# Kernel tuning notes

Hardware: AMD Instinct MI355X
Metric: run time of the kernel (lower is better)

## Reference

```python
import jax, jax.numpy as jnp
import numpy as np

N, E, B = 65536, 262144, 2048   # nodes, edges, graphs
ND, ED, H, L = 32, 8, 128, 4    # node feat, edge feat, hidden, egnn layers
PE, PH, CH = 1280, 512, 512     # protein embed, protein hidden, combined hidden
EPS = 1e-8


def _seg_mean(data, ids, num):
    s = jax.ops.segment_sum(data, ids, num_segments=num)
    c = jax.ops.segment_sum(jnp.ones((data.shape[0], 1), data.dtype), ids, num_segments=num)
    return s / jnp.clip(c, 1.0)


def setup_inputs() -> dict:
    key = jax.random.key(0)
    ks = iter(jax.random.split(key, 40))

    def p(shape, scale=0.05):
        return jax.random.normal(next(ks), shape, dtype=jnp.float32) * scale

    inp = {
        "x": jax.random.normal(next(ks), (N, ND), dtype=jnp.float32),
        "pos": jax.random.normal(next(ks), (N, 3), dtype=jnp.float32),
        "edge_attr": jax.random.uniform(next(ks), (E, ED), dtype=jnp.float32),
        "protein_embedding": jax.random.normal(next(ks), (B, PE), dtype=jnp.float32),
        "edge_index": jax.random.randint(next(ks), (2, E), 0, N),
        "batch": jnp.arange(N, dtype=jnp.int64) // (N // B),
        # EGNN embeddings
        "emb_in_w": p((ND, H)), "emb_in_b": p((H,)),
        "emb_out_w": p((H, H)), "emb_out_b": p((H,)),
        # per-layer stacked params (leading dim L)
        "edge_w1": p((L, 2 * H + 1 + ED, H)), "edge_b1": p((L, H)),
        "edge_w2": p((L, H, H)), "edge_b2": p((L, H)),
        "att_w": p((L, H, 1)), "att_b": p((L, 1)),
        "coord_w1": p((L, H, H)), "coord_b1": p((L, H)),
        "coord_w2": p((L, H, 1)),  # no bias, xavier in torch impl
        "node_w1": p((L, 2 * H, H)), "node_b1": p((L, H)),
        "node_w2": p((L, H, H)), "node_b2": p((L, H)),
        # protein + combined heads
        "prot_w": p((PE, PH)), "prot_b": p((PH,)),
        "comb_w1": p((H + PH, CH)), "comb_b1": p((CH,)),
        "comb_w2": p((CH, 1)), "comb_b2": p((1,)),
    }
    return inp


def _forward(x, pos, edge_attr, protein_embedding,
             emb_in_w, emb_in_b, emb_out_w, emb_out_b,
             edge_w1, edge_b1, edge_w2, edge_b2, att_w, att_b,
             coord_w1, coord_b1, coord_w2,
             node_w1, node_b1, node_w2, node_b2,
             prot_w, prot_b, comb_w1, comb_b1, comb_w2, comb_b2,
             edge_index, batch):
    row, col = edge_index[0], edge_index[1]
    h = x @ emb_in_w + emb_in_b
    for l in range(L):
        # coord2radial (normalize=True)
        d = pos[row] - pos[col]                       # [E,3]
        radial = jnp.sum(d * d, axis=-1, keepdims=True)  # [E,1]
        d = d / (jnp.sqrt(radial) + EPS)
        # edge model with sigmoid attention gate
        e_in = jnp.concatenate([h[row], h[col], radial, edge_attr], axis=-1)
        m = jax.nn.silu(e_in @ edge_w1[l] + edge_b1[l])
        m = jax.nn.silu(m @ edge_w2[l] + edge_b2[l])
        m = m * jax.nn.sigmoid(m @ att_w[l] + att_b[l])
        # coord model (tanh=True, coords_agg='mean')
        t = jax.nn.silu(m @ coord_w1[l] + coord_b1[l])
        trans = d * jnp.tanh(t @ coord_w2[l])         # [E,3]
        pos = pos + _seg_mean(trans, row, N)
        # node model (sum aggregation, residual)
        agg = jax.ops.segment_sum(m, row, num_segments=N)
        nh = jax.nn.silu(jnp.concatenate([h, agg], axis=-1) @ node_w1[l] + node_b1[l])
        h = h + (nh @ node_w2[l] + node_b2[l])
    h = h @ emb_out_w + emb_out_b
    # global mean pool over graphs
    drug = _seg_mean(h, batch, B)                     # [B,H]
    prot = jax.nn.relu(protein_embedding @ prot_w + prot_b)  # dropout = identity (eval)
    c = jnp.concatenate([drug, prot], axis=-1)
    c = jax.nn.relu(c @ comb_w1 + comb_b1)
    logits = (c @ comb_w2 + comb_b2)[:, 0]
    return logits


def reference(x, pos, edge_attr, protein_embedding,
              emb_in_w, emb_in_b, emb_out_w, emb_out_b,
              edge_w1, edge_b1, edge_w2, edge_b2, att_w, att_b,
              coord_w1, coord_b1, coord_w2,
              node_w1, node_b1, node_w2, node_b2,
              prot_w, prot_b, comb_w1, comb_b1, comb_w2, comb_b2,
              edge_index, batch):
    logits = _forward(x, pos, edge_attr, protein_embedding,
                      emb_in_w, emb_in_b, emb_out_w, emb_out_b,
                      edge_w1, edge_b1, edge_w2, edge_b2, att_w, att_b,
                      coord_w1, coord_b1, coord_w2,
                      node_w1, node_b1, node_w2, node_b2,
                      prot_w, prot_b, comb_w1, comb_b1, comb_w2, comb_b2,
                      edge_index, batch)
    attention_weights = jnp.zeros((B, 1, 1), dtype=logits.dtype)
    return logits, attention_weights
```

## Files before the change

kernel.cpp:

```cpp
#include <hip/hip_runtime.h>
#include <math.h>


static constexpr int NN  = 65536;
static constexpr int NE  = 262144;
static constexpr int NB  = 2048;
static constexpr int NDF = 32;
static constexpr int HD  = 128;
static constexpr int NL  = 4;
static constexpr int PED = 1280;
static constexpr int PHD = 512;
static constexpr int CHD = 512;
static constexpr float EPSV = 1e-8f;

static constexpr int KK1 = 9;
static constexpr int KK2 = 4;
static constexpr int KKN1 = 8;
static constexpr int KKP = 40;
static constexpr int KKC = 20;

static constexpr int ES = 36;

typedef __attribute__((ext_vector_type(8))) short bf8_t;
typedef __attribute__((ext_vector_type(4))) float f4_t;

__device__ __forceinline__ float sigmoid_f(float x) {
  return __fdividef(1.0f, 1.0f + __expf(-x));
}
__device__ __forceinline__ float silu_f(float x) { return x * sigmoid_f(x); }

__device__ __forceinline__ ushort f2bf(float f) {
  unsigned u = __float_as_uint(f);
  u += 0x7FFFu + ((u >> 16) & 1u);
  return (ushort)(u >> 16);
}
__device__ __forceinline__ float bf2f(ushort h) {
  return __uint_as_float(((unsigned)h) << 16);
}
__device__ __forceinline__ unsigned pk2bf(float a, float b) {
  return (unsigned)f2bf(a) | ((unsigned)f2bf(b) << 16);
}

__device__ __forceinline__ void fma44(float (&acc)[4][4], const float4 a, const float4 w) {
  const float av[4] = {a.x, a.y, a.z, a.w};
  const float wv[4] = {w.x, w.y, w.z, w.w};
#pragma unroll
  for (int i = 0; i < 4; ++i)
#pragma unroll
    for (int j = 0; j < 4; ++j) acc[i][j] = fmaf(av[i], wv[j], acc[i][j]);
}


__global__ void hist_kernel(const int* __restrict__ ei, int* __restrict__ deg) {
  const int e = blockIdx.x * 256 + threadIdx.x;
  if (e < NE) atomicAdd(&deg[ei[e]], 1);
}

__global__ __launch_bounds__(1024) void scan_kernel(const int* __restrict__ deg,
                                                    int* __restrict__ row_ptr) {
  __shared__ int wsums[16];
  __shared__ int carry_s;
  const int t = threadIdx.x;
  const int lane = t & 63, wave = t >> 6;
  if (t == 0) { carry_s = 0; row_ptr[0] = 0; }
  __syncthreads();
  for (int c = 0; c < NN / 1024; ++c) {
    const int i = c * 1024 + t;
    int incl = deg[i];
#pragma unroll
    for (int d = 1; d < 64; d <<= 1) {
      const int u = __shfl_up(incl, d, 64);
      if (lane >= d) incl += u;
    }
    if (lane == 63) wsums[wave] = incl;
    __syncthreads();
    if (t == 0) {
      int a = carry_s;
#pragma unroll
      for (int w = 0; w < 16; ++w) { const int tmp = wsums[w]; wsums[w] = a; a += tmp; }
      carry_s = a;
    }
    __syncthreads();
    row_ptr[i + 1] = wsums[wave] + incl;
    __syncthreads();
  }
}

__global__ void fill_kernel(const int* __restrict__ ei, const int* __restrict__ row_ptr,
                            int* __restrict__ fill_pos, int* __restrict__ edge_ids) {
  const int e = blockIdx.x * 256 + threadIdx.x;
  if (e < NE) {
    const int n = ei[e];
    const int s = atomicAdd(&fill_pos[n], 1);
    edge_ids[row_ptr[n] + s] = e;
  }
}

__global__ void perm_kernel(const int* __restrict__ ei, const int* __restrict__ edge_ids,
                            const float* __restrict__ edge_attr,
                            int* __restrict__ rowp, int* __restrict__ colp,
                            float* __restrict__ eap) {
  const int i = blockIdx.x * 256 + threadIdx.x;
  if (i >= NE) return;
  const int e = edge_ids[i];
  rowp[i] = ei[e];
  colp[i] = ei[NE + e];
  const float4 a = *(const float4*)(edge_attr + (size_t)e * 8);
  const float4 b = *(const float4*)(edge_attr + (size_t)e * 8 + 4);
  *(float4*)(eap + (size_t)i * 8) = a;
  *(float4*)(eap + (size_t)i * 8 + 4) = b;
}

__global__ void pos_copy_kernel(const float* __restrict__ pos, float* __restrict__ pc) {
  const int n = blockIdx.x * 256 + threadIdx.x;
  if (n < NN) {
    const float4 v = make_float4(pos[(size_t)n * 3 + 0], pos[(size_t)n * 3 + 1],
                                 pos[(size_t)n * 3 + 2], 0.0f);
    *(float4*)(pc + (size_t)n * 4) = v;
  }
}


__global__ __launch_bounds__(256) void packw_kernel(
    const float* __restrict__ W, ushort* __restrict__ Wp,
    int K, int N, int KK, size_t sW, size_t sWp) {
  const int layer = blockIdx.y;
  const int NTG = N >> 4;
  const int i = blockIdx.x * 256 + threadIdx.x;
  if (i >= KK * NTG * 64) return;
  const int l = i & 63;
  const int q = i >> 6;
  const int ntg = q % NTG;
  const int kk = q / NTG;
  const int k0 = kk * 32 + ((l >> 4) * 8);
  const int n = ntg * 16 + (l & 15);
  const float* w = W + layer * sW;
  unsigned ww[4];
#pragma unroll
  for (int p = 0; p < 4; ++p) {
    const int ka = k0 + p * 2, kb = ka + 1;
    const unsigned lo = (ka < K) ? f2bf(w[(size_t)ka * N + n]) : 0;
    const unsigned hi = (kb < K) ? f2bf(w[(size_t)kb * N + n]) : 0;
    ww[p] = lo | (hi << 16);
  }
  *(uint4*)(Wp + layer * sWp + (size_t)i * 8) = make_uint4(ww[0], ww[1], ww[2], ww[3]);
}

__global__ __launch_bounds__(256) void cvt_bf_kernel(const float* __restrict__ in,
                                                     ushort* __restrict__ out, int n) {
  const int i = blockIdx.x * 256 + threadIdx.x;
  if (i * 8 >= n) return;
  const float4 v0 = *(const float4*)(in + (size_t)i * 8);
  const float4 v1 = *(const float4*)(in + (size_t)i * 8 + 4);
  *(uint4*)(out + (size_t)i * 8) =
      make_uint4(pk2bf(v0.x, v0.y), pk2bf(v0.z, v0.w), pk2bf(v1.x, v1.y), pk2bf(v1.z, v1.w));
}


__global__ __launch_bounds__(256) void geom_kernel(
    const float* __restrict__ pos_cur, const float* __restrict__ eap,
    const int* __restrict__ rowp, const int* __restrict__ colp,
    float* __restrict__ dnb, ushort* __restrict__ extra) {
  const int i = blockIdx.x * 256 + threadIdx.x;
  if (i >= NE) return;
  const int r = rowp[i], c = colp[i];
  const float4 pr = *(const float4*)(pos_cur + (size_t)r * 4);
  const float4 pc = *(const float4*)(pos_cur + (size_t)c * 4);
  const float dx = pr.x - pc.x, dy = pr.y - pc.y, dz = pr.z - pc.z;
  const float radial = dx * dx + dy * dy + dz * dz;
  const float inv = 1.0f / (sqrtf(radial) + EPSV);
  *(float4*)(dnb + (size_t)i * 4) = make_float4(dx * inv, dy * inv, dz * inv, 0.0f);
  const float4 ea0 = *(const float4*)(eap + (size_t)i * 8);
  const float4 ea1 = *(const float4*)(eap + (size_t)i * 8 + 4);
  ushort* dst = extra + (size_t)i * 32;
  *(uint4*)(dst) = make_uint4(pk2bf(radial, ea0.x), pk2bf(ea0.y, ea0.z),
                              pk2bf(ea0.w, ea1.x), pk2bf(ea1.y, ea1.z));
  *(uint4*)(dst + 8)  = make_uint4((unsigned)f2bf(ea1.w), 0, 0, 0);
  *(uint4*)(dst + 16) = make_uint4(0, 0, 0, 0);
  *(uint4*)(dst + 24) = make_uint4(0, 0, 0, 0);
}


__global__ __launch_bounds__(256) void emb_in_kernel(
    const float* __restrict__ x, const float* __restrict__ W,
    const float* __restrict__ B, float* __restrict__ h, ushort* __restrict__ hbf) {
  __shared__ float xs[NDF * ES];
  const int t = threadIdx.x;
  const int n0 = blockIdx.x * 32;
  {
    const int r = t >> 3;
    const int kq = (t & 7) * 4;
    const float4 v = *(const float4*)(x + (size_t)(n0 + r) * NDF + kq);
    xs[(kq + 0) * ES + r] = v.x;
    xs[(kq + 1) * ES + r] = v.y;
    xs[(kq + 2) * ES + r] = v.z;
    xs[(kq + 3) * ES + r] = v.w;
  }
  __syncthreads();
  const int eg = t & 7, fg = t >> 3;
  float acc[4][4] = {};
  const float* wp = W + fg * 4;
#pragma unroll
  for (int k = 0; k < NDF; ++k) {
    const float4 a = *(const float4*)&xs[k * ES + eg * 4];
    const float4 w = *(const float4*)(wp + (size_t)k * HD);
    fma44(acc, a, w);
  }
  const float4 bv = *(const float4*)(B + fg * 4);
  const float bb[4] = {bv.x, bv.y, bv.z, bv.w};
#pragma unroll
  for (int i = 0; i < 4; ++i) {
    const float4 o = make_float4(acc[i][0] + bb[0], acc[i][1] + bb[1],
                                 acc[i][2] + bb[2], acc[i][3] + bb[3]);
    *(float4*)(h + (size_t)(n0 + eg * 4 + i) * HD + fg * 4) = o;
    *(uint2*)(hbf + (size_t)(n0 + eg * 4 + i) * HD + fg * 4) =
        make_uint2(pk2bf(o.x, o.y), pk2bf(o.z, o.w));
  }
}


__global__ __launch_bounds__(256) void edge_mfma_kernel(
    const ushort* __restrict__ hbf, const ushort* __restrict__ extra,
    const int* __restrict__ rowp, const int* __restrict__ colp,
    const float* __restrict__ dnb,
    const ushort* __restrict__ W1p, const float* __restrict__ B1,
    const ushort* __restrict__ W2p, const float* __restrict__ B2,
    const float* __restrict__ AW, const float* __restrict__ AB,
    const ushort* __restrict__ CW1p, const float* __restrict__ CB1,
    const float* __restrict__ CW2,
    ushort* __restrict__ m_bf, float* __restrict__ trans_out) {
  __shared__ ushort mtileT[64 * 128];
  __shared__ int ridx[64], cidx[64];
  __shared__ float redbuf[2][64];
  __shared__ float gates[64];

  const int t = threadIdx.x;
  const int e0 = blockIdx.x * 64;
  if (t < 64) {
    ridx[t] = rowp[e0 + t];
    cidx[t] = colp[e0 + t];
  }
  __syncthreads();

  const int w = t >> 6, l = t & 63;
  const int wn = w & 1, we = w >> 1;
  const int g = l >> 4, ln = l & 15;
  const int nb = wn * 64;
  const int eb = we * 32;

  int je[2], er[2], ec[2], swz[2];
#pragma unroll
  for (int et = 0; et < 2; ++et) {
    je[et] = eb + et * 16 + ln;
    er[et] = ridx[je[et]];
    ec[et] = cidx[je[et]];
    swz[et] = (je[et] & 7) << 3;
  }

  const f4_t zf = {0.0f, 0.0f, 0.0f, 0.0f};
  f4_t acc[4][2];
#pragma unroll
  for (int mt = 0; mt < 4; ++mt)
#pragma unroll
    for (int et = 0; et < 2; ++et) acc[mt][et] = zf;

#pragma unroll
  for (int kk = 0; kk < KK1; ++kk) {
    bf8_t aw[4], be[2];
#pragma unroll
    for (int mt = 0; mt < 4; ++mt)
      aw[mt] = *(const bf8_t*)(W1p + ((size_t)(kk * 8 + wn * 4 + mt) * 64 + l) * 8);
#pragma unroll
    for (int et = 0; et < 2; ++et) {
      if (kk < 8) {
        const int idx = (kk < 4) ? er[et] : ec[et];
        be[et] = *(const bf8_t*)(hbf + (size_t)idx * HD + (kk & 3) * 32 + g * 8);
      } else {
        be[et] = *(const bf8_t*)(extra + (size_t)(e0 + je[et]) * 32 + g * 8);
      }
    }
#pragma unroll
    for (int mt = 0; mt < 4; ++mt)
#pragma unroll
      for (int et = 0; et < 2; ++et)
        acc[mt][et] = __builtin_amdgcn_mfma_f32_16x16x32_bf16(aw[mt], be[et], acc[mt][et], 0, 0, 0);
  }

  {
#pragma unroll
    for (int mt = 0; mt < 4; ++mt) {
      const int n0 = nb + mt * 16 + g * 4;
      const float4 bv = *(const float4*)(B1 + n0);
#pragma unroll
      for (int et = 0; et < 2; ++et) {
        const unsigned lo = pk2bf(silu_f(acc[mt][et][0] + bv.x), silu_f(acc[mt][et][1] + bv.y));
        const unsigned hi = pk2bf(silu_f(acc[mt][et][2] + bv.z), silu_f(acc[mt][et][3] + bv.w));
        *(uint2*)&mtileT[je[et] * HD + (n0 ^ swz[et])] = make_uint2(lo, hi);
      }
    }
  }
  __syncthreads();

  f4_t acc2[4][2];
#pragma unroll
  for (int mt = 0; mt < 4; ++mt)
#pragma unroll
    for (int et = 0; et < 2; ++et) acc2[mt][et] = zf;
#pragma unroll
  for (int kk = 0; kk < KK2; ++kk) {
    bf8_t aw[4], be[2];
#pragma unroll
    for (int mt = 0; mt < 4; ++mt)
      aw[mt] = *(const bf8_t*)(W2p + ((size_t)(kk * 8 + wn * 4 + mt) * 64 + l) * 8);
    const int nk = kk * 32 + g * 8;
#pragma unroll
    for (int et = 0; et < 2; ++et)
      be[et] = *(const bf8_t*)&mtileT[je[et] * HD + (nk ^ swz[et])];
#pragma unroll
    for (int mt = 0; mt < 4; ++mt)
#pragma unroll
      for (int et = 0; et < 2; ++et)
        acc2[mt][et] = __builtin_amdgcn_mfma_f32_16x16x32_bf16(aw[mt], be[et], acc2[mt][et], 0, 0, 0);
  }

  float m2v[4][2][4];
  {
    float p[2] = {0.0f, 0.0f};
#pragma unroll
    for (int mt = 0; mt < 4; ++mt) {
      const int n0 = nb + mt * 16 + g * 4;
      const float4 bv = *(const float4*)(B2 + n0);
      const float4 av = *(const float4*)(AW + n0);
      const float bb[4] = {bv.x, bv.y, bv.z, bv.w};
      const float aa[4] = {av.x, av.y, av.z, av.w};
#pragma unroll
      for (int et = 0; et < 2; ++et)
#pragma unroll
        for (int r = 0; r < 4; ++r) {
          const float v = silu_f(acc2[mt][et][r] + bb[r]);
          m2v[mt][et][r] = v;
          p[et] = fmaf(v, aa[r], p[et]);
        }
    }
#pragma unroll
    for (int et = 0; et < 2; ++et) {
      p[et] += __shfl_xor(p[et], 16, 64);
      p[et] += __shfl_xor(p[et], 32, 64);
    }
    if (l < 16) {
#pragma unroll
      for (int et = 0; et < 2; ++et) redbuf[wn][eb + et * 16 + l] = p[et];
    }
  }
  __syncthreads();
  if (t < 64) gates[t] = sigmoid_f(redbuf[0][t] + redbuf[1][t] + AB[0]);
  __syncthreads();

  {
    float grow[2];
#pragma unroll
    for (int et = 0; et < 2; ++et) grow[et] = gates[je[et]];
#pragma unroll
    for (int mt = 0; mt < 4; ++mt) {
      const int n0 = nb + mt * 16 + g * 4;
#pragma unroll
      for (int et = 0; et < 2; ++et) {
        const unsigned lo = pk2bf(m2v[mt][et][0] * grow[et], m2v[mt][et][1] * grow[et]);
        const unsigned hi = pk2bf(m2v[mt][et][2] * grow[et], m2v[mt][et][3] * grow[et]);
        *(uint2*)&mtileT[je[et] * HD + (n0 ^ swz[et])] = make_uint2(lo, hi);
      }
    }
  }
  __syncthreads();

  f4_t acc3[4][2];
#pragma unroll
  for (int mt = 0; mt < 4; ++mt)
#pragma unroll
    for (int et = 0; et < 2; ++et) acc3[mt][et] = zf;
#pragma unroll
  for (int kk = 0; kk < KK2; ++kk) {
    bf8_t aw[4], be[2];
#pragma unroll
    for (int mt = 0; mt < 4; ++mt)
      aw[mt] = *(const bf8_t*)(CW1p + ((size_t)(kk * 8 + wn * 4 + mt) * 64 + l) * 8);
    const int nk = kk * 32 + g * 8;
#pragma unroll
    for (int et = 0; et < 2; ++et)
      be[et] = *(const bf8_t*)&mtileT[je[et] * HD + (nk ^ swz[et])];
#pragma unroll
    for (int mt = 0; mt < 4; ++mt)
#pragma unroll
      for (int et = 0; et < 2; ++et)
        acc3[mt][et] = __builtin_amdgcn_mfma_f32_16x16x32_bf16(aw[mt], be[et], acc3[mt][et], 0, 0, 0);
  }
  {
    float q[2] = {0.0f, 0.0f};
#pragma unroll
    for (int mt = 0; mt < 4; ++mt) {
      const int n0 = nb + mt * 16 + g * 4;
      const float4 bv = *(const float4*)(CB1 + n0);
      const float4 cv = *(const float4*)(CW2 + n0);
      const float bb[4] = {bv.x, bv.y, bv.z, bv.w};
      const float cc[4] = {cv.x, cv.y, cv.z, cv.w};
#pragma unroll
      for (int et = 0; et < 2; ++et)
#pragma unroll
        for (int r = 0; r < 4; ++r)
          q[et] = fmaf(silu_f(acc3[mt][et][r] + bb[r]), cc[r], q[et]);
    }
#pragma unroll
    for (int et = 0; et < 2; ++et) {
      q[et] += __shfl_xor(q[et], 16, 64);
      q[et] += __shfl_xor(q[et], 32, 64);
    }
    if (l < 16) {
#pragma unroll
      for (int et = 0; et < 2; ++et) redbuf[wn][eb + et * 16 + l] = q[et];
    }
  }
  __syncthreads();
  if (t < 64) {
    const float s = tanhf(redbuf[0][t] + redbuf[1][t]);
    const f4_t dn = *(const f4_t*)(dnb + (size_t)(e0 + t) * 4);
    const f4_t tr = dn * s;
    *(f4_t*)(trans_out + (size_t)(e0 + t) * 4) = tr;
  }

#pragma unroll
  for (int it = 0; it < 4; ++it) {
    const int i = it * 256 + t;
    const int row = i >> 4;
    const int c8 = (i & 15) * 8;
    const uint4 v = *(const uint4*)&mtileT[row * HD + (c8 ^ ((row & 7) << 3))];
    *(uint4*)(m_bf + (size_t)(e0 + row) * HD + c8) = v;
  }
}


__global__ __launch_bounds__(256) void gather_kernel(
    const ushort* __restrict__ m_bf, const float* __restrict__ trans,
    const int* __restrict__ row_ptr,
    ushort* __restrict__ agg_bf, float* __restrict__ pos_cur) {
  const int t = threadIdx.x;
  const int wave = t >> 6, lane = t & 63;
  const int n = blockIdx.x * 4 + wave;
  const int s = row_ptr[n], e_end = row_ptr[n + 1];
  float a0 = 0.0f, a1 = 0.0f, ta = 0.0f;
  for (int i = s; i < e_end; ++i) {
    const ushort2 v = *(const ushort2*)(m_bf + (size_t)i * HD + lane * 2);
    a0 += bf2f(v.x);
    a1 += bf2f(v.y);
    if (lane < 4) ta += trans[(size_t)i * 4 + lane];
  }
  ushort2 ab;
  ab.x = f2bf(a0);
  ab.y = f2bf(a1);
  *(ushort2*)(agg_bf + (size_t)n * HD + lane * 2) = ab;
  if (lane < 3) {
    const int dg = e_end - s;
    pos_cur[(size_t)n * 4 + lane] += ta / (float)(dg > 0 ? dg : 1);
  }
}


__global__ __launch_bounds__(256) void node_mfma_kernel(
    float* __restrict__ h, const ushort* __restrict__ hbf,
    const ushort* __restrict__ agg_bf,
    const ushort* __restrict__ W1p, const float* __restrict__ B1,
    const ushort* __restrict__ W2p, const float* __restrict__ B2,
    ushort* __restrict__ hbf_out) {
  __shared__ ushort mtileT[64 * 128];
  const int t = threadIdx.x;
  const int n0blk = blockIdx.x * 64;
  const int w = t >> 6, l = t & 63;
  const int wn = w & 1, we = w >> 1;
  const int g = l >> 4, ln = l & 15;
  const int nb = wn * 64;
  const int eb = we * 32;

  int jn[2], swz[2];
#pragma unroll
  for (int et = 0; et < 2; ++et) {
    jn[et] = eb + et * 16 + ln;
    swz[et] = (jn[et] & 7) << 3;
  }

  const f4_t zf = {0.0f, 0.0f, 0.0f, 0.0f};
  f4_t acc[4][2];
#pragma unroll
  for (int mt = 0; mt < 4; ++mt)
#pragma unroll
    for (int et = 0; et < 2; ++et) acc[mt][et] = zf;

#pragma unroll
  for (int kk = 0; kk < KKN1; ++kk) {
    bf8_t aw[4], be[2];
#pragma unroll
    for (int mt = 0; mt < 4; ++mt)
      aw[mt] = *(const bf8_t*)(W1p + ((size_t)(kk * 8 + wn * 4 + mt) * 64 + l) * 8);
#pragma unroll
    for (int et = 0; et < 2; ++et) {
      const size_t base = (size_t)(n0blk + jn[et]) * HD + (kk & 3) * 32 + g * 8;
      be[et] = (kk < 4) ? *(const bf8_t*)(hbf + base) : *(const bf8_t*)(agg_bf + base);
    }
#pragma unroll
    for (int mt = 0; mt < 4; ++mt)
#pragma unroll
      for (int et = 0; et < 2; ++et)
        acc[mt][et] = __builtin_amdgcn_mfma_f32_16x16x32_bf16(aw[mt], be[et], acc[mt][et], 0, 0, 0);
  }
  {
#pragma unroll
    for (int mt = 0; mt < 4; ++mt) {
      const int n0 = nb + mt * 16 + g * 4;
      const float4 bv = *(const float4*)(B1 + n0);
#pragma unroll
      for (int et = 0; et < 2; ++et) {
        const unsigned lo = pk2bf(silu_f(acc[mt][et][0] + bv.x), silu_f(acc[mt][et][1] + bv.y));
        const unsigned hi = pk2bf(silu_f(acc[mt][et][2] + bv.z), silu_f(acc[mt][et][3] + bv.w));
        *(uint2*)&mtileT[jn[et] * HD + (n0 ^ swz[et])] = make_uint2(lo, hi);
      }
    }
  }
  __syncthreads();

  f4_t acc2[4][2];
#pragma unroll
  for (int mt = 0; mt < 4; ++mt)
#pragma unroll
    for (int et = 0; et < 2; ++et) acc2[mt][et] = zf;
#pragma unroll
  for (int kk = 0; kk < KK2; ++kk) {
    bf8_t aw[4], be[2];
#pragma unroll
    for (int mt = 0; mt < 4; ++mt)
      aw[mt] = *(const bf8_t*)(W2p + ((size_t)(kk * 8 + wn * 4 + mt) * 64 + l) * 8);
    const int nk = kk * 32 + g * 8;
#pragma unroll
    for (int et = 0; et < 2; ++et)
      be[et] = *(const bf8_t*)&mtileT[jn[et] * HD + (nk ^ swz[et])];
#pragma unroll
    for (int mt = 0; mt < 4; ++mt)
#pragma unroll
      for (int et = 0; et < 2; ++et)
        acc2[mt][et] = __builtin_amdgcn_mfma_f32_16x16x32_bf16(aw[mt], be[et], acc2[mt][et], 0, 0, 0);
  }
  {
#pragma unroll
    for (int mt = 0; mt < 4; ++mt) {
      const int n0 = nb + mt * 16 + g * 4;
      const float4 bv = *(const float4*)(B2 + n0);
#pragma unroll
      for (int et = 0; et < 2; ++et) {
        float* hp = h + (size_t)(n0blk + jn[et]) * HD + n0;
        const float4 old = *(const float4*)hp;
        float4 o;
        o.x = old.x + acc2[mt][et][0] + bv.x;
        o.y = old.y + acc2[mt][et][1] + bv.y;
        o.z = old.z + acc2[mt][et][2] + bv.z;
        o.w = old.w + acc2[mt][et][3] + bv.w;
        *(float4*)hp = o;
        *(uint2*)(hbf_out + (size_t)(n0blk + jn[et]) * HD + n0) =
            make_uint2(pk2bf(o.x, o.y), pk2bf(o.z, o.w));
      }
    }
  }
}


__global__ __launch_bounds__(256) void gemm_head_kernel(
    const ushort* __restrict__ A, const ushort* __restrict__ Wp,
    const float* __restrict__ bias, ushort* __restrict__ out,
    int lda, int KK, int NTG, int ldo, int col_off) {
  const int t = threadIdx.x;
  const int rb = blockIdx.x * 64;
  const int cb = blockIdx.y * 128;
  const int w = t >> 6, l = t & 63;
  const int wr = w >> 1, wc = w & 1;
  const int g = l >> 4, ln = l & 15;
  const int row0 = wr * 32;
  int rowA[2];
#pragma unroll
  for (int mt = 0; mt < 2; ++mt) rowA[mt] = row0 + mt * 16 + ln;

  const f4_t zf = {0.0f, 0.0f, 0.0f, 0.0f};
  f4_t acc[2][4];
#pragma unroll
  for (int mt = 0; mt < 2; ++mt)
#pragma unroll
    for (int nt = 0; nt < 4; ++nt) acc[mt][nt] = zf;

  const int ntg0 = (cb >> 4) + wc * 4;
  for (int kk = 0; kk < KK; ++kk) {
    bf8_t a[2], b[4];
#pragma unroll
    for (int mt = 0; mt < 2; ++mt)
      a[mt] = *(const bf8_t*)(A + (size_t)(rb + rowA[mt]) * lda + kk * 32 + g * 8);
#pragma unroll
    for (int nt = 0; nt < 4; ++nt)
      b[nt] = *(const bf8_t*)(Wp + ((size_t)(kk * NTG + ntg0 + nt) * 64 + l) * 8);
#pragma unroll
    for (int mt = 0; mt < 2; ++mt)
#pragma unroll
      for (int nt = 0; nt < 4; ++nt)
        acc[mt][nt] = __builtin_amdgcn_mfma_f32_16x16x32_bf16(a[mt], b[nt], acc[mt][nt], 0, 0, 0);
  }
  {
    float bn[4];
#pragma unroll
    for (int nt = 0; nt < 4; ++nt) bn[nt] = bias[cb + wc * 64 + nt * 16 + ln];
#pragma unroll
    for (int mt = 0; mt < 2; ++mt)
#pragma unroll
      for (int nt = 0; nt < 4; ++nt) {
        const int col = cb + wc * 64 + nt * 16 + ln;
#pragma unroll
        for (int r = 0; r < 4; ++r) {
          const int row = row0 + mt * 16 + g * 4 + r;
          const float v = fmaxf(acc[mt][nt][r] + bn[nt], 0.0f);
          out[(size_t)(rb + row) * ldo + col_off + col] = f2bf(v);
        }
      }
  }
}


__global__ __launch_bounds__(128) void pool_kernel(
    const float* __restrict__ h, const float* __restrict__ W,
    const float* __restrict__ B, ushort* __restrict__ c_in) {
  __shared__ float mh[HD];
  const int g = blockIdx.x, t = threadIdx.x;
  float s = 0.0f;
#pragma unroll 4
  for (int n = 0; n < 32; ++n) s += h[((size_t)g * 32 + n) * HD + t];
  mh[t] = s * (1.0f / 32.0f);
  __syncthreads();
  float acc = B[t];
#pragma unroll 4
  for (int k = 0; k < HD; ++k) acc = fmaf(mh[k], W[(size_t)k * HD + t], acc);
  c_in[(size_t)g * (HD + PHD) + t] = f2bf(acc);
}

__global__ __launch_bounds__(256) void logits_kernel(
    const ushort* __restrict__ c, const float* __restrict__ w2,
    const float* __restrict__ b2, float* __restrict__ out) {
  const int t = threadIdx.x;
  const int wave = t >> 6, lane = t & 63;
  const int r = blockIdx.x * 4 + wave;
  const ushort* cp = c + (size_t)r * CHD + lane * 8;
  const float* wp = w2 + lane * 8;
  float s = 0.0f;
#pragma unroll
  for (int j = 0; j < 8; ++j) s = fmaf(bf2f(cp[j]), wp[j], s);
#pragma unroll
  for (int off = 32; off > 0; off >>= 1) s += __shfl_down(s, off, 64);
  if (lane == 0) {
    out[r] = s + b2[0];
    out[NB + r] = 0.0f;
  }
}


extern "C" void kernel_launch(void* const* d_in, const int* in_sizes, int n_in,
                              void* d_out, int out_size, void* d_ws, size_t ws_size,
                              hipStream_t stream) {
  const float* x          = (const float*)d_in[0];
  const float* pos        = (const float*)d_in[1];
  const float* edge_attr  = (const float*)d_in[2];
  const float* pe         = (const float*)d_in[3];
  const int*   edge_index = (const int*)d_in[4];
  const float* emb_in_w   = (const float*)d_in[6];
  const float* emb_in_b   = (const float*)d_in[7];
  const float* emb_out_w  = (const float*)d_in[8];
  const float* emb_out_b  = (const float*)d_in[9];
  const float* edge_w1    = (const float*)d_in[10];
  const float* edge_b1    = (const float*)d_in[11];
  const float* edge_w2    = (const float*)d_in[12];
  const float* edge_b2    = (const float*)d_in[13];
  const float* att_w      = (const float*)d_in[14];
  const float* att_b      = (const float*)d_in[15];
  const float* coord_w1   = (const float*)d_in[16];
  const float* coord_b1   = (const float*)d_in[17];
  const float* coord_w2   = (const float*)d_in[18];
  const float* node_w1    = (const float*)d_in[19];
  const float* node_b1    = (const float*)d_in[20];
  const float* node_w2    = (const float*)d_in[21];
  const float* node_b2    = (const float*)d_in[22];
  const float* prot_w     = (const float*)d_in[23];
  const float* prot_b     = (const float*)d_in[24];
  const float* comb_w1    = (const float*)d_in[25];
  const float* comb_b1    = (const float*)d_in[26];
  const float* comb_w2    = (const float*)d_in[27];
  const float* comb_b2    = (const float*)d_in[28];
  float* out = (float*)d_out;
  (void)in_sizes; (void)n_in; (void)out_size; (void)ws_size;

  char* ws = (char*)d_ws;
  size_t off = 0;
  auto carve = [&](size_t bytes) -> void* {
    void* p = ws + off;
    off += (bytes + 255) & ~(size_t)255;
    return p;
  };
  float*  h       = (float*)carve((size_t)NN * HD * 4);
  ushort* h_bf    = (ushort*)carve((size_t)NN * HD * 2);
  ushort* agg_bf  = (ushort*)carve((size_t)NN * HD * 2);
  ushort* m_bf    = (ushort*)carve((size_t)NE * HD * 2);
  float*  trans   = (float*)carve((size_t)NE * 4 * 4);
  float*  dnb     = (float*)carve((size_t)NE * 4 * 4);
  ushort* extra   = (ushort*)carve((size_t)NE * 32 * 2);
  float*  eap     = (float*)carve((size_t)NE * 8 * 4);
  float*  pos_cur = (float*)carve((size_t)NN * 4 * 4);
  ushort* pe_bf   = (ushort*)carve((size_t)NB * PED * 2);
  ushort* c_in    = (ushort*)carve((size_t)NB * (HD + PHD) * 2);
  ushort* c1      = (ushort*)carve((size_t)NB * CHD * 2);
  const size_t sW1p  = (size_t)KK1 * 8 * 64 * 8;
  const size_t sW2p  = (size_t)KK2 * 8 * 64 * 8;
  const size_t sNW1p = (size_t)KKN1 * 8 * 64 * 8;
  const size_t sPWp  = (size_t)KKP * 32 * 64 * 8;
  const size_t sCWp  = (size_t)KKC * 32 * 64 * 8;
  ushort* W1p     = (ushort*)carve(sW1p * NL * 2);
  ushort* W2p     = (ushort*)carve(sW2p * NL * 2);
  ushort* CW1p    = (ushort*)carve(sW2p * NL * 2);
  ushort* NW1p    = (ushort*)carve(sNW1p * NL * 2);
  ushort* NW2p    = (ushort*)carve(sW2p * NL * 2);
  ushort* PWp     = (ushort*)carve(sPWp * 2);
  ushort* CWp     = (ushort*)carve(sCWp * 2);
  int* deg        = (int*)carve((size_t)NN * 4);
  int* row_ptr    = (int*)carve((size_t)(NN + 1) * 4);
  int* fill_pos   = (int*)carve((size_t)NN * 4);
  int* edge_ids   = (int*)carve((size_t)NE * 4);
  int* rowp       = (int*)carve((size_t)NE * 4);
  int* colp       = (int*)carve((size_t)NE * 4);

  hipMemsetAsync(deg, 0, (size_t)NN * 4, stream);
  hipMemsetAsync(fill_pos, 0, (size_t)NN * 4, stream);

  pos_copy_kernel<<<NN / 256, 256, 0, stream>>>(pos, pos_cur);
  hist_kernel<<<NE / 256, 256, 0, stream>>>(edge_index, deg);
  scan_kernel<<<1, 1024, 0, stream>>>(deg, row_ptr);
  fill_kernel<<<NE / 256, 256, 0, stream>>>(edge_index, row_ptr, fill_pos, edge_ids);
  perm_kernel<<<NE / 256, 256, 0, stream>>>(edge_index, edge_ids, edge_attr,
                                            rowp, colp, eap);

  packw_kernel<<<dim3(18, NL), 256, 0, stream>>>(edge_w1, W1p, 265, HD, KK1,
                                                 (size_t)265 * HD, sW1p);
  packw_kernel<<<dim3(8, NL), 256, 0, stream>>>(edge_w2, W2p, HD, HD, KK2,
                                                (size_t)HD * HD, sW2p);
  packw_kernel<<<dim3(8, NL), 256, 0, stream>>>(coord_w1, CW1p, HD, HD, KK2,
                                                (size_t)HD * HD, sW2p);
  packw_kernel<<<dim3(16, NL), 256, 0, stream>>>(node_w1, NW1p, 2 * HD, HD, KKN1,
                                                 (size_t)2 * HD * HD, sNW1p);
  packw_kernel<<<dim3(8, NL), 256, 0, stream>>>(node_w2, NW2p, HD, HD, KK2,
                                                (size_t)HD * HD, sW2p);
  packw_kernel<<<dim3(320, 1), 256, 0, stream>>>(prot_w, PWp, PED, PHD, KKP, 0, 0);
  packw_kernel<<<dim3(160, 1), 256, 0, stream>>>(comb_w1, CWp, HD + PHD, CHD, KKC, 0, 0);

  cvt_bf_kernel<<<NB * PED / (256 * 8), 256, 0, stream>>>(pe, pe_bf, NB * PED);

  emb_in_kernel<<<NN / 32, 256, 0, stream>>>(x, emb_in_w, emb_in_b, h, h_bf);

  for (int l = 0; l < NL; ++l) {
    geom_kernel<<<NE / 256, 256, 0, stream>>>(pos_cur, eap, rowp, colp, dnb, extra);
    edge_mfma_kernel<<<NE / 64, 256, 0, stream>>>(
        h_bf, extra, rowp, colp, dnb,
        W1p + (size_t)l * sW1p, edge_b1 + (size_t)l * HD,
        W2p + (size_t)l * sW2p, edge_b2 + (size_t)l * HD,
        att_w + (size_t)l * HD, att_b + l,
        CW1p + (size_t)l * sW2p, coord_b1 + (size_t)l * HD,
        coord_w2 + (size_t)l * HD,
        m_bf, trans);
    gather_kernel<<<NN / 4, 256, 0, stream>>>(m_bf, trans, row_ptr, agg_bf, pos_cur);
    node_mfma_kernel<<<NN / 64, 256, 0, stream>>>(
        h, h_bf, agg_bf,
        NW1p + (size_t)l * sNW1p, node_b1 + (size_t)l * HD,
        NW2p + (size_t)l * sW2p, node_b2 + (size_t)l * HD, h_bf);
  }

  pool_kernel<<<NB, 128, 0, stream>>>(h, emb_out_w, emb_out_b, c_in);
  gemm_head_kernel<<<dim3(NB / 64, PHD / 128), 256, 0, stream>>>(
      pe_bf, PWp, prot_b, c_in, PED, KKP, PHD / 16, HD + PHD, HD);
  gemm_head_kernel<<<dim3(NB / 64, CHD / 128), 256, 0, stream>>>(
      c_in, CWp, comb_b1, c1, HD + PHD, KKC, CHD / 16, CHD, 0);
  logits_kernel<<<NB / 4, 256, 0, stream>>>(c1, comb_w2, comb_b2, out);
}
```

Before: 1.026 ms.

## Parallelize CSR scan, prebuild edge-attr tile once, use hardware bf16 pack

Replaces the single-block serial prefix scan with a two-kernel scan (per-chunk sums, then block-parallel scan). Edge attributes are converted to bf16 and written into the padded extra buffer once, in the permutation kernel, so each layer's geom kernel writes only the radial term instead of re-reading fp32 attributes and rewriting the whole row. pk2bf now uses the v_cvt_pk_bf16_f32 instruction, which may round slightly differently from the software rounding. The edge kernel block index is also remapped in an interleaved pattern, presumably to change locality across XCDs.

```diff
diff --git a/kernel.cpp b/kernel.cpp
--- a/kernel.cpp
+++ b/kernel.cpp
@@ -38,7 +38,9 @@
   return __uint_as_float(((unsigned)h) << 16);
 }
 __device__ __forceinline__ unsigned pk2bf(float a, float b) {
-  return (unsigned)f2bf(a) | ((unsigned)f2bf(b) << 16);
+  unsigned r;
+  asm("v_cvt_pk_bf16_f32 %0, %1, %2" : "=v"(r) : "v"(a), "v"(b));
+  return r;
 }
 
 __device__ __forceinline__ void fma44(float (&acc)[4][4], const float4 a, const float4 w) {
@@ -56,34 +58,51 @@
   if (e < NE) atomicAdd(&deg[ei[e]], 1);
 }
 
-__global__ __launch_bounds__(1024) void scan_kernel(const int* __restrict__ deg,
-                                                    int* __restrict__ row_ptr) {
-  __shared__ int wsums[16];
-  __shared__ int carry_s;
+__global__ __launch_bounds__(256) void scan1_kernel(const int* __restrict__ deg,
+                                                    int* __restrict__ cbase) {
+  __shared__ int wsum[4];
   const int t = threadIdx.x;
   const int lane = t & 63, wave = t >> 6;
-  if (t == 0) { carry_s = 0; row_ptr[0] = 0; }
-  __syncthreads();
-  for (int c = 0; c < NN / 1024; ++c) {
-    const int i = c * 1024 + t;
-    int incl = deg[i];
-#pragma unroll
-    for (int d = 1; d < 64; d <<= 1) {
-      const int u = __shfl_up(incl, d, 64);
-      if (lane >= d) incl += u;
-    }
-    if (lane == 63) wsums[wave] = incl;
-    __syncthreads();
-    if (t == 0) {
-      int a = carry_s;
-#pragma unroll
-      for (int w = 0; w < 16; ++w) { const int tmp = wsums[w]; wsums[w] = a; a += tmp; }
-      carry_s = a;
-    }
-    __syncthreads();
-    row_ptr[i + 1] = wsums[wave] + incl;
-    __syncthreads();
-  }
+  int s = 0;
+  const int4* p = (const int4*)deg + (size_t)t * 64;
+#pragma unroll 8
+  for (int j = 0; j < 64; ++j) {
+    const int4 v = p[j];
+    s += v.x + v.y + v.z + v.w;
+  }
+  int incl = s;
+#pragma unroll
+  for (int d = 1; d < 64; d <<= 1) {
+    const int u = __shfl_up(incl, d, 64);
+    if (lane >= d) incl += u;
+  }
+  if (lane == 63) wsum[wave] = incl;
+  __syncthreads();
+  int base = 0;
+  for (int w2 = 0; w2 < wave; ++w2) base += wsum[w2];
+  cbase[t] = base + incl - s;
+}
+
+__global__ __launch_bounds__(256) void scan2_kernel(const int* __restrict__ deg,
+                                                    const int* __restrict__ cbase,
+                                                    int* __restrict__ row_ptr) {
+  __shared__ int wsum[4];
+  const int b = blockIdx.x, t = threadIdx.x;
+  const int lane = t & 63, wave = t >> 6;
+  const int i = b * 256 + t;
+  const int s = deg[i];
+  int incl = s;
+#pragma unroll
+  for (int d = 1; d < 64; d <<= 1) {
+    const int u = __shfl_up(incl, d, 64);
+    if (lane >= d) incl += u;
+  }
+  if (lane == 63) wsum[wave] = incl;
+  __syncthreads();
+  int base = cbase[b];
+  for (int w2 = 0; w2 < wave; ++w2) base += wsum[w2];
+  row_ptr[i + 1] = base + incl;
+  if (i == 0) row_ptr[0] = 0;
 }
 
 __global__ void fill_kernel(const int* __restrict__ ei, const int* __restrict__ row_ptr,
@@ -99,7 +118,7 @@
 __global__ void perm_kernel(const int* __restrict__ ei, const int* __restrict__ edge_ids,
                             const float* __restrict__ edge_attr,
                             int* __restrict__ rowp, int* __restrict__ colp,
-                            float* __restrict__ eap) {
+                            ushort* __restrict__ extra) {
   const int i = blockIdx.x * 256 + threadIdx.x;
   if (i >= NE) return;
   const int e = edge_ids[i];
@@ -107,8 +126,12 @@
   colp[i] = ei[NE + e];
   const float4 a = *(const float4*)(edge_attr + (size_t)e * 8);
   const float4 b = *(const float4*)(edge_attr + (size_t)e * 8 + 4);
-  *(float4*)(eap + (size_t)i * 8) = a;
-  *(float4*)(eap + (size_t)i * 8 + 4) = b;
+  ushort* dst = extra + (size_t)i * 32;
+  *(uint4*)(dst) = make_uint4(pk2bf(0.0f, a.x), pk2bf(a.y, a.z),
+                              pk2bf(a.w, b.x), pk2bf(b.y, b.z));
+  *(uint4*)(dst + 8)  = make_uint4(pk2bf(b.w, 0.0f), 0, 0, 0);
+  *(uint4*)(dst + 16) = make_uint4(0, 0, 0, 0);
+  *(uint4*)(dst + 24) = make_uint4(0, 0, 0, 0);
 }
 
 __global__ void pos_copy_kernel(const float* __restrict__ pos, float* __restrict__ pc) {
@@ -158,7 +181,7 @@
 
 
 __global__ __launch_bounds__(256) void geom_kernel(
-    const float* __restrict__ pos_cur, const float* __restrict__ eap,
+    const float* __restrict__ pos_cur,
     const int* __restrict__ rowp, const int* __restrict__ colp,
     float* __restrict__ dnb, ushort* __restrict__ extra) {
   const int i = blockIdx.x * 256 + threadIdx.x;
@@ -170,14 +193,7 @@
   const float radial = dx * dx + dy * dy + dz * dz;
   const float inv = 1.0f / (sqrtf(radial) + EPSV);
   *(float4*)(dnb + (size_t)i * 4) = make_float4(dx * inv, dy * inv, dz * inv, 0.0f);
-  const float4 ea0 = *(const float4*)(eap + (size_t)i * 8);
-  const float4 ea1 = *(const float4*)(eap + (size_t)i * 8 + 4);
-  ushort* dst = extra + (size_t)i * 32;
-  *(uint4*)(dst) = make_uint4(pk2bf(radial, ea0.x), pk2bf(ea0.y, ea0.z),
-                              pk2bf(ea0.w, ea1.x), pk2bf(ea1.y, ea1.z));
-  *(uint4*)(dst + 8)  = make_uint4((unsigned)f2bf(ea1.w), 0, 0, 0);
-  *(uint4*)(dst + 16) = make_uint4(0, 0, 0, 0);
-  *(uint4*)(dst + 24) = make_uint4(0, 0, 0, 0);
+  extra[(size_t)i * 32] = f2bf(radial);
 }
 
 
@@ -235,7 +251,8 @@
   __shared__ float gates[64];
 
   const int t = threadIdx.x;
-  const int e0 = blockIdx.x * 64;
+  const int bid = blockIdx.x;
+  const int e0 = ((bid & 7) * (NE / 64 / 8) + (bid >> 3)) * 64;
   if (t < 64) {
     ridx[t] = rowp[e0 + t];
     cidx[t] = colp[e0 + t];
@@ -286,17 +303,15 @@
         acc[mt][et] = __builtin_amdgcn_mfma_f32_16x16x32_bf16(aw[mt], be[et], acc[mt][et], 0, 0, 0);
   }
 
-  {
-#pragma unroll
-    for (int mt = 0; mt < 4; ++mt) {
-      const int n0 = nb + mt * 16 + g * 4;
-      const float4 bv = *(const float4*)(B1 + n0);
-#pragma unroll
-      for (int et = 0; et < 2; ++et) {
-        const unsigned lo = pk2bf(silu_f(acc[mt][et][0] + bv.x), silu_f(acc[mt][et][1] + bv.y));
-        const unsigned hi = pk2bf(silu_f(acc[mt][et][2] + bv.z), silu_f(acc[mt][et][3] + bv.w));
-        *(uint2*)&mtileT[je[et] * HD + (n0 ^ swz[et])] = make_uint2(lo, hi);
-      }
+#pragma unroll
+  for (int mt = 0; mt < 4; ++mt) {
+    const int n0 = nb + mt * 16 + g * 4;
+    const float4 bv = *(const float4*)(B1 + n0);
+#pragma unroll
+    for (int et = 0; et < 2; ++et) {
+      const unsigned lo = pk2bf(silu_f(acc[mt][et][0] + bv.x), silu_f(acc[mt][et][1] + bv.y));
+      const unsigned hi = pk2bf(silu_f(acc[mt][et][2] + bv.z), silu_f(acc[mt][et][3] + bv.w));
+      *(uint2*)&mtileT[je[et] * HD + (n0 ^ swz[et])] = make_uint2(lo, hi);
     }
   }
   __syncthreads();
@@ -453,10 +468,7 @@
     a1 += bf2f(v.y);
     if (lane < 4) ta += trans[(size_t)i * 4 + lane];
   }
-  ushort2 ab;
-  ab.x = f2bf(a0);
-  ab.y = f2bf(a1);
-  *(ushort2*)(agg_bf + (size_t)n * HD + lane * 2) = ab;
+  *(unsigned*)(agg_bf + (size_t)n * HD + lane * 2) = pk2bf(a0, a1);
   if (lane < 3) {
     const int dg = e_end - s;
     pos_cur[(size_t)n * 4 + lane] += ta / (float)(dg > 0 ? dg : 1);
@@ -510,17 +522,15 @@
       for (int et = 0; et < 2; ++et)
         acc[mt][et] = __builtin_amdgcn_mfma_f32_16x16x32_bf16(aw[mt], be[et], acc[mt][et], 0, 0, 0);
   }
-  {
-#pragma unroll
-    for (int mt = 0; mt < 4; ++mt) {
-      const int n0 = nb + mt * 16 + g * 4;
-      const float4 bv = *(const float4*)(B1 + n0);
-#pragma unroll
-      for (int et = 0; et < 2; ++et) {
-        const unsigned lo = pk2bf(silu_f(acc[mt][et][0] + bv.x), silu_f(acc[mt][et][1] + bv.y));
-        const unsigned hi = pk2bf(silu_f(acc[mt][et][2] + bv.z), silu_f(acc[mt][et][3] + bv.w));
-        *(uint2*)&mtileT[jn[et] * HD + (n0 ^ swz[et])] = make_uint2(lo, hi);
-      }
+#pragma unroll
+  for (int mt = 0; mt < 4; ++mt) {
+    const int n0 = nb + mt * 16 + g * 4;
+    const float4 bv = *(const float4*)(B1 + n0);
+#pragma unroll
+    for (int et = 0; et < 2; ++et) {
+      const unsigned lo = pk2bf(silu_f(acc[mt][et][0] + bv.x), silu_f(acc[mt][et][1] + bv.y));
+      const unsigned hi = pk2bf(silu_f(acc[mt][et][2] + bv.z), silu_f(acc[mt][et][3] + bv.w));
+      *(uint2*)&mtileT[jn[et] * HD + (n0 ^ swz[et])] = make_uint2(lo, hi);
     }
   }
   __syncthreads();
@@ -546,24 +556,22 @@
       for (int et = 0; et < 2; ++et)
         acc2[mt][et] = __builtin_amdgcn_mfma_f32_16x16x32_bf16(aw[mt], be[et], acc2[mt][et], 0, 0, 0);
   }
-  {
-#pragma unroll
-    for (int mt = 0; mt < 4; ++mt) {
-      const int n0 = nb + mt * 16 + g * 4;
-      const float4 bv = *(const float4*)(B2 + n0);
-#pragma unroll
-      for (int et = 0; et < 2; ++et) {
-        float* hp = h + (size_t)(n0blk + jn[et]) * HD + n0;
-        const float4 old = *(const float4*)hp;
-        float4 o;
-        o.x = old.x + acc2[mt][et][0] + bv.x;
-        o.y = old.y + acc2[mt][et][1] + bv.y;
-        o.z = old.z + acc2[mt][et][2] + bv.z;
-        o.w = old.w + acc2[mt][et][3] + bv.w;
-        *(float4*)hp = o;
-        *(uint2*)(hbf_out + (size_t)(n0blk + jn[et]) * HD + n0) =
-            make_uint2(pk2bf(o.x, o.y), pk2bf(o.z, o.w));
-      }
+#pragma unroll
+  for (int mt = 0; mt < 4; ++mt) {
+    const int n0 = nb + mt * 16 + g * 4;
+    const float4 bv = *(const float4*)(B2 + n0);
+#pragma unroll
+    for (int et = 0; et < 2; ++et) {
+      float* hp = h + (size_t)(n0blk + jn[et]) * HD + n0;
+      const float4 old = *(const float4*)hp;
+      float4 o;
+      o.x = old.x + acc2[mt][et][0] + bv.x;
+      o.y = old.y + acc2[mt][et][1] + bv.y;
+      o.z = old.z + acc2[mt][et][2] + bv.z;
+      o.w = old.w + acc2[mt][et][3] + bv.w;
+      *(float4*)hp = o;
+      *(uint2*)(hbf_out + (size_t)(n0blk + jn[et]) * HD + n0) =
+          make_uint2(pk2bf(o.x, o.y), pk2bf(o.z, o.w));
     }
   }
 }
@@ -710,7 +718,6 @@
   float*  trans   = (float*)carve((size_t)NE * 4 * 4);
   float*  dnb     = (float*)carve((size_t)NE * 4 * 4);
   ushort* extra   = (ushort*)carve((size_t)NE * 32 * 2);
-  float*  eap     = (float*)carve((size_t)NE * 8 * 4);
   float*  pos_cur = (float*)carve((size_t)NN * 4 * 4);
   ushort* pe_bf   = (ushort*)carve((size_t)NB * PED * 2);
   ushort* c_in    = (ushort*)carve((size_t)NB * (HD + PHD) * 2);
@@ -733,16 +740,18 @@
   int* edge_ids   = (int*)carve((size_t)NE * 4);
   int* rowp       = (int*)carve((size_t)NE * 4);
   int* colp       = (int*)carve((size_t)NE * 4);
+  int* cbase      = (int*)carve((size_t)256 * 4);
 
   hipMemsetAsync(deg, 0, (size_t)NN * 4, stream);
   hipMemsetAsync(fill_pos, 0, (size_t)NN * 4, stream);
 
   pos_copy_kernel<<<NN / 256, 256, 0, stream>>>(pos, pos_cur);
   hist_kernel<<<NE / 256, 256, 0, stream>>>(edge_index, deg);
-  scan_kernel<<<1, 1024, 0, stream>>>(deg, row_ptr);
+  scan1_kernel<<<1, 256, 0, stream>>>(deg, cbase);
+  scan2_kernel<<<NN / 256, 256, 0, stream>>>(deg, cbase, row_ptr);
   fill_kernel<<<NE / 256, 256, 0, stream>>>(edge_index, row_ptr, fill_pos, edge_ids);
   perm_kernel<<<NE / 256, 256, 0, stream>>>(edge_index, edge_ids, edge_attr,
-                                            rowp, colp, eap);
+                                            rowp, colp, extra);
 
   packw_kernel<<<dim3(18, NL), 256, 0, stream>>>(edge_w1, W1p, 265, HD, KK1,
                                                  (size_t)265 * HD, sW1p);
@@ -762,7 +771,7 @@
   emb_in_kernel<<<NN / 32, 256, 0, stream>>>(x, emb_in_w, emb_in_b, h, h_bf);
 
   for (int l = 0; l < NL; ++l) {
-    geom_kernel<<<NE / 256, 256, 0, stream>>>(pos_cur, eap, rowp, colp, dnb, extra);
+    geom_kernel<<<NE / 256, 256, 0, stream>>>(pos_cur, rowp, colp, dnb, extra);
     edge_mfma_kernel<<<NE / 64, 256, 0, stream>>>(
         h_bf, extra, rowp, colp, dnb,
         W1p + (size_t)l * sW1p, edge_b1 + (size_t)l * HD,
```

Result: faster. 966.4 us (-5.8%).
